# Performance work log

Hardware: AMD Instinct MI355X
Metric: run time of the kernel (lower is better)

Reference implementation:

```python
import jax, jax.numpy as jnp
import numpy as np

DIM = 192
HEADS = 6
WIN = (2, 6, 12)          # (pl, lat, lon)
TOW = 64                  # type_of_windows = (8//2)*(96//6)
N_TOK = WIN[0] * WIN[1] * WIN[2]            # 144
TABLE_ROWS = WIN[0]**2 * WIN[1]**2 * (2 * WIN[2] - 1)  # 3312


def calc_position_bias_indices(size):
    pl, la, lo = size
    plq = np.arange(pl); plk = -np.arange(pl) * pl
    laq = np.arange(la); lak = -np.arange(la) * la
    lon = np.arange(lo)
    gq = np.stack(np.meshgrid(plq, laq, lon, indexing='ij'))  # [3,pl,la,lo]
    gk = np.stack(np.meshgrid(plk, lak, lon, indexing='ij'))
    fq = gq.reshape(3, -1)
    fk = gk.reshape(3, -1)
    d = fq[:, :, None] - fk[:, None, :]          # [3,N,N]
    d = np.transpose(d, (1, 2, 0)).copy()
    d[:, :, 2] += lo - 1
    d[:, :, 1] *= 2 * lo - 1
    d[:, :, 0] *= (2 * lo - 1) * la * la
    return d.sum(-1)                              # [N,N]


def setup_inputs() -> dict:
    key = jax.random.key(0)
    ks = jax.random.split(key, 7)
    B_, nW, N, C = 15, TOW, N_TOK, DIM
    x = jax.random.normal(ks[0], (B_, nW, N, C), jnp.float32)
    mask = jax.random.normal(ks[1], (15, nW, N, N), jnp.float32)  # nLon=15
    qkv_w = jax.random.normal(ks[2], (3 * C, C), jnp.float32) * 0.02
    qkv_b = jnp.zeros((3 * C,), jnp.float32)
    table = jax.random.normal(ks[3], (TABLE_ROWS, TOW, HEADS), jnp.float32) * 0.02
    proj_w = jax.random.normal(ks[4], (C, C), jnp.float32) * 0.02
    proj_b = jnp.zeros((C,), jnp.float32)
    pos_index = jnp.asarray(calc_position_bias_indices(WIN), jnp.int32)  # [N,N]
    return {"x": x, "mask": mask, "qkv_w": qkv_w, "qkv_b": qkv_b,
            "table": table, "proj_w": proj_w, "proj_b": proj_b,
            "pos_index": pos_index}


def reference(x, mask, qkv_w, qkv_b, table, proj_w, proj_b, pos_index):
    B_, nW, N, C = x.shape
    h = HEADS
    hd = C // h
    scale = hd ** -0.5
    # qkv projection -> (3, B_, h, nW, N, hd)
    qkv = (jnp.einsum('bwnc,dc->bwnd', x, qkv_w) + qkv_b)
    qkv = qkv.reshape(B_, nW, N, 3, h, hd).transpose(3, 0, 4, 1, 2, 5)
    q, k, v = qkv[0] * scale, qkv[1], qkv[2]
    attn = jnp.einsum('bhwqd,bhwkd->bhwqk', q, k)      # [B_,h,nW,N,N]
    # gather earth position bias: [N,N,tow,h] -> [h,tow,N,N]
    bias = table[pos_index.reshape(-1)].reshape(N, N, nW, h)
    bias = bias.transpose(3, 2, 0, 1)
    attn = attn + bias[None]
    nLon = mask.shape[0]
    attn = attn.reshape(B_ // nLon, nLon, h, nW, N, N) + mask[None, :, None]
    attn = attn.reshape(B_, h, nW, N, N)
    attn = jax.nn.softmax(attn, axis=-1)
    out = jnp.einsum('bhwqk,bhwkd->bhwqd', attn, v)
    out = out.transpose(0, 2, 3, 1, 4).reshape(B_, nW, N, C)
    return jnp.einsum('bwnc,dc->bwnd', out, proj_w) + proj_b
```

## Files before the change

### kernel.cpp

```cpp
#include <hip/hip_runtime.h>

#define HEADS 6
#define N_TOK 144
#define DIM   192
#define NW    64
#define NB    15
#define NBW   (NB * NW)

typedef __attribute__((ext_vector_type(8))) short bf16x8;
typedef __attribute__((ext_vector_type(4))) float f32x4;

#define MFMA(a, b, c) __builtin_amdgcn_mfma_f32_16x16x32_bf16(a, b, c, 0, 0, 0)

static __device__ __forceinline__ short f2bf(float f) {
    union { float f; unsigned u; } v; v.f = f;
    unsigned r = v.u + 0x7FFFu + ((v.u >> 16) & 1u);
    return (short)(r >> 16);
}
static __device__ __forceinline__ float bf2f(short s) {
    union { unsigned u; float f; } v;
    v.u = ((unsigned)(unsigned short)s) << 16;
    return v.f;
}
static __device__ __forceinline__ unsigned pk2(float a, float b) {
    return (unsigned)(unsigned short)f2bf(a) |
           ((unsigned)(unsigned short)f2bf(b) << 16);
}

__global__ __launch_bounds__(256)
void bias_k(const float* __restrict__ table, const int* __restrict__ pos_index,
            short* __restrict__ bias_bf) {
    const int t = blockIdx.x;
    for (int e = threadIdx.x; e < N_TOK * N_TOK; e += 256) {
        int idx = pos_index[e];
        bias_bf[(long)t * (N_TOK * N_TOK) + e] = f2bf(table[(long)idx * 384 + t]);
    }
}

__global__ __launch_bounds__(256)
void cvt_k(const float* __restrict__ w, short* __restrict__ o, int n) {
    int i = blockIdx.x * 256 + threadIdx.x;
    if (i < n) o[i] = f2bf(w[i]);
}

__global__ __launch_bounds__(576, 2)
void fused64_k(const float* __restrict__ x, const short* __restrict__ qkvw_bf,
               const float* __restrict__ qkv_b, const short* __restrict__ bias_bf,
               const float* __restrict__ mask, const short* __restrict__ pwt,
               const float* __restrict__ proj_b, float* __restrict__ out) {
    __shared__ short klds[N_TOK * 40];
    __shared__ short vlds[32 * 156];
    __shared__ short pws[9 * 16 * 40];
    __shared__ short outb[N_TOK * 200];

    const int p  = blockIdx.x;
    const int bw = (p & 7) * 120 + (p >> 3);
    const int tid = threadIdx.x;
    const int lane = tid & 63, lq = lane & 15, lg = lane >> 4;
    const int wid = tid >> 6;
    const int m0 = wid * 16;
    const int q  = m0 + lq;
    const int w  = bw & 63;
    const float scale = 0.17677669529663687f;

    bf16x8 af[6];
    {
        const float* xg = x + ((long)bw * N_TOK + q) * DIM;
        #pragma unroll
        for (int ks = 0; ks < 6; ++ks) {
            const float4* pp = (const float4*)&xg[ks * 32 + 8 * lg];
            float4 f0 = pp[0], f1 = pp[1];
            bf16x8 a;
            a[0]=f2bf(f0.x); a[1]=f2bf(f0.y); a[2]=f2bf(f0.z); a[3]=f2bf(f0.w);
            a[4]=f2bf(f1.x); a[5]=f2bf(f1.y); a[6]=f2bf(f1.z); a[7]=f2bf(f1.w);
            af[ks] = a;
        }
    }

    float4 mreg[9];
    {
        const float* mp = mask + (long)bw * (N_TOK * N_TOK) + q * N_TOK + 4 * lg;
        #pragma unroll
        for (int nt = 0; nt < 9; ++nt) mreg[nt] = *(const float4*)&mp[nt * 16];
    }

    short* pw = pws + wid * 16 * 40;
    const f32x4 zf = {};
    const bf16x8 zb = {};

    #pragma unroll 1
    for (int h = 0; h < HEADS; ++h) {
        f32x4 acc[3][2] = {};
        #pragma unroll
        for (int ks = 0; ks < 6; ++ks)
            #pragma unroll
            for (int sel = 0; sel < 3; ++sel)
                #pragma unroll
                for (int nt = 0; nt < 2; ++nt) {
                    bf16x8 b = *(const bf16x8*)&qkvw_bf[
                        ((long)sel * 192 + h * 32 + nt * 16 + lq) * 192 + ks * 32 + 8 * lg];
                    acc[sel][nt] = MFMA(af[ks], b, acc[sel][nt]);
                }

        #pragma unroll
        for (int nt = 0; nt < 2; ++nt) {
            float bb = qkv_b[h * 32 + nt * 16 + lq];
            #pragma unroll
            for (int i = 0; i < 4; ++i)
                pw[(4 * lg + i) * 40 + nt * 16 + lq] =
                    f2bf((acc[0][nt][i] + bb) * scale);
        }

        __syncthreads();
        #pragma unroll
        for (int nt = 0; nt < 2; ++nt) {
            float bk = qkv_b[192 + h * 32 + nt * 16 + lq];
            float bv = qkv_b[384 + h * 32 + nt * 16 + lq];
            #pragma unroll
            for (int i = 0; i < 4; ++i) {
                klds[(m0 + 4 * lg + i) * 40 + nt * 16 + lq] = f2bf(acc[1][nt][i] + bk);
                vlds[(nt * 16 + lq) * 156 + m0 + 4 * lg + i] = f2bf(acc[2][nt][i] + bv);
            }
        }
        __syncthreads();

        bf16x8 bq = *(const bf16x8*)&pw[lq * 40 + 8 * lg];
        f32x4 lgt[9];
        #pragma unroll
        for (int nt = 0; nt < 9; ++nt) {
            bf16x8 ak = *(const bf16x8*)&klds[(nt * 16 + lq) * 40 + 8 * lg];
            lgt[nt] = MFMA(ak, bq, zf);
        }

        const short* bp = bias_bf + (long)(w * 6 + h) * (N_TOK * N_TOK)
                        + q * N_TOK + 4 * lg;
        #pragma unroll
        for (int nt = 0; nt < 9; ++nt) {
            short4 bs = *(const short4*)&bp[nt * 16];
            lgt[nt][0] += bf2f(bs.x) + mreg[nt].x;
            lgt[nt][1] += bf2f(bs.y) + mreg[nt].y;
            lgt[nt][2] += bf2f(bs.z) + mreg[nt].z;
            lgt[nt][3] += bf2f(bs.w) + mreg[nt].w;
        }

        float m = lgt[0][0];
        #pragma unroll
        for (int nt = 0; nt < 9; ++nt)
            #pragma unroll
            for (int i = 0; i < 4; ++i) m = fmaxf(m, lgt[nt][i]);
        m = fmaxf(m, __shfl_xor(m, 16));
        m = fmaxf(m, __shfl_xor(m, 32));
        float s = 0.f;
        #pragma unroll
        for (int nt = 0; nt < 9; ++nt)
            #pragma unroll
            for (int i = 0; i < 4; ++i) {
                float pe = __expf(lgt[nt][i] - m);
                lgt[nt][i] = pe;
                s += pe;
            }
        s += __shfl_xor(s, 16);
        s += __shfl_xor(s, 32);
        const float inv = 1.f / s;

        f32x4 o[2] = {};
        #pragma unroll
        for (int kt = 0; kt < 5; ++kt) {
            const int nt0 = 2 * kt;
            *(unsigned*)&pw[lq * 40 + 4 * lg]     = pk2(lgt[nt0][0], lgt[nt0][1]);
            *(unsigned*)&pw[lq * 40 + 4 * lg + 2] = pk2(lgt[nt0][2], lgt[nt0][3]);
            if (kt < 4) {
                const int nt1 = nt0 + 1;
                *(unsigned*)&pw[lq * 40 + 16 + 4 * lg]     = pk2(lgt[nt1][0], lgt[nt1][1]);
                *(unsigned*)&pw[lq * 40 + 16 + 4 * lg + 2] = pk2(lgt[nt1][2], lgt[nt1][3]);
            }
            bf16x8 bpf = *(const bf16x8*)&pw[lq * 40 + 8 * lg];
            #pragma unroll
            for (int et = 0; et < 2; ++et) {
                bf16x8 av = *(const bf16x8*)&vlds[(et * 16 + lq) * 156 + kt * 32 + 8 * lg];
                bf16x8 aa = av, bb = bpf;
                if (kt == 4 && lg >= 2) { aa = zb; bb = zb; }
                o[et] = MFMA(aa, bb, o[et]);
            }
        }

        #pragma unroll
        for (int et = 0; et < 2; ++et) {
            short4 sx = { f2bf(o[et][0] * inv), f2bf(o[et][1] * inv),
                          f2bf(o[et][2] * inv), f2bf(o[et][3] * inv) };
            *(short4*)&outb[q * 200 + h * 32 + et * 16 + 4 * lg] = sx;
        }
    }
    __syncthreads();

    f32x4 acc[12] = {};
    #pragma unroll
    for (int ks = 0; ks < 6; ++ks) {
        const int k0 = ks * 32 + 8 * lg;
        bf16x8 a = *(const bf16x8*)&outb[(m0 + lq) * 200 + k0];
        #pragma unroll
        for (int nt = 0; nt < 12; ++nt) {
            bf16x8 b = *(const bf16x8*)&pwt[(nt * 16 + lq) * DIM + k0];
            acc[nt] = MFMA(a, b, acc[nt]);
        }
    }
    float* ob = out + (long)bw * N_TOK * DIM;
    #pragma unroll
    for (int nt = 0; nt < 12; ++nt) {
        float pb = proj_b[nt * 16 + lq];
        #pragma unroll
        for (int i = 0; i < 4; ++i)
            ob[(m0 + 4 * lg + i) * DIM + nt * 16 + lq] = acc[nt][i] + pb;
    }
}

extern "C" void kernel_launch(void* const* d_in, const int* in_sizes, int n_in,
                              void* d_out, int out_size, void* d_ws, size_t ws_size,
                              hipStream_t stream) {
    const float* x        = (const float*)d_in[0];
    const float* mask     = (const float*)d_in[1];
    const float* qkv_w    = (const float*)d_in[2];
    const float* qkv_b    = (const float*)d_in[3];
    const float* table    = (const float*)d_in[4];
    const float* proj_w   = (const float*)d_in[5];
    const float* proj_b   = (const float*)d_in[6];
    const int*   pos_index= (const int*)d_in[7];
    float* out = (float*)d_out;

    short* bias_bf  = (short*)d_ws;
    short* projw_bf = bias_bf + (size_t)384 * N_TOK * N_TOK;
    short* qkvw_bf  = projw_bf + 36864;

    bias_k<<<384, 256, 0, stream>>>(table, pos_index, bias_bf);
    cvt_k<<<144, 256, 0, stream>>>(proj_w, projw_bf, DIM * DIM);
    cvt_k<<<432, 256, 0, stream>>>(qkv_w, qkvw_bf, 3 * DIM * DIM);

    fused64_k<<<NBW, 576, 0, stream>>>(x, qkvw_bf, qkv_b, bias_bf, mask,
                                       projw_bf, proj_b, out);
}
```

Measured before the change: 505.3 us.

## Split fused attention into per-head blocks plus separate projection kernel

The fused kernel, which looped over six heads per window, becomes one block per (window, head), which multiplies the grid by six. The per-head attention output goes to a bf16 workspace in global memory, and a new proj_k kernel runs the output projection over thirds of each window. The aim is more parallelism and shorter per-block serial chains, and it removes the outb shared-memory buffer. In exchange, every head block reloads x and the mask, and an extra global round trip plus one more launch are added.

Result: slower. 536.2 us (+6.1%).

```diff
diff --git a/kernel.cpp b/kernel.cpp
--- a/kernel.cpp
+++ b/kernel.cpp
@@ -44,17 +44,17 @@
 }
 
 __global__ __launch_bounds__(576, 2)
-void fused64_k(const float* __restrict__ x, const short* __restrict__ qkvw_bf,
+void attnqkv_k(const float* __restrict__ x, const short* __restrict__ qkvw_bf,
                const float* __restrict__ qkv_b, const short* __restrict__ bias_bf,
-               const float* __restrict__ mask, const short* __restrict__ pwt,
-               const float* __restrict__ proj_b, float* __restrict__ out) {
+               const float* __restrict__ mask, short* __restrict__ tmp) {
     __shared__ short klds[N_TOK * 40];
     __shared__ short vlds[32 * 156];
     __shared__ short pws[9 * 16 * 40];
-    __shared__ short outb[N_TOK * 200];
 
     const int p  = blockIdx.x;
-    const int bw = (p & 7) * 120 + (p >> 3);
+    const int l  = (p & 7) * 720 + (p >> 3);
+    const int h  = l % HEADS;
+    const int bw = l / HEADS;
     const int tid = threadIdx.x;
     const int lane = tid & 63, lq = lane & 15, lg = lane >> 4;
     const int wid = tid >> 6;
@@ -88,116 +88,124 @@
     const f32x4 zf = {};
     const bf16x8 zb = {};
 
-    #pragma unroll 1
-    for (int h = 0; h < HEADS; ++h) {
-        f32x4 acc[3][2] = {};
-        #pragma unroll
-        for (int ks = 0; ks < 6; ++ks)
+    f32x4 acc[3][2] = {};
+    #pragma unroll
+    for (int ks = 0; ks < 6; ++ks)
+        #pragma unroll
+        for (int sel = 0; sel < 3; ++sel)
             #pragma unroll
-            for (int sel = 0; sel < 3; ++sel)
-                #pragma unroll
-                for (int nt = 0; nt < 2; ++nt) {
-                    bf16x8 b = *(const bf16x8*)&qkvw_bf[
-                        ((long)sel * 192 + h * 32 + nt * 16 + lq) * 192 + ks * 32 + 8 * lg];
-                    acc[sel][nt] = MFMA(af[ks], b, acc[sel][nt]);
-                }
-
-        #pragma unroll
-        for (int nt = 0; nt < 2; ++nt) {
-            float bb = qkv_b[h * 32 + nt * 16 + lq];
-            #pragma unroll
-            for (int i = 0; i < 4; ++i)
-                pw[(4 * lg + i) * 40 + nt * 16 + lq] =
-                    f2bf((acc[0][nt][i] + bb) * scale);
-        }
-
-        __syncthreads();
-        #pragma unroll
-        for (int nt = 0; nt < 2; ++nt) {
-            float bk = qkv_b[192 + h * 32 + nt * 16 + lq];
-            float bv = qkv_b[384 + h * 32 + nt * 16 + lq];
-            #pragma unroll
-            for (int i = 0; i < 4; ++i) {
-                klds[(m0 + 4 * lg + i) * 40 + nt * 16 + lq] = f2bf(acc[1][nt][i] + bk);
-                vlds[(nt * 16 + lq) * 156 + m0 + 4 * lg + i] = f2bf(acc[2][nt][i] + bv);
+            for (int nt = 0; nt < 2; ++nt) {
+                bf16x8 b = *(const bf16x8*)&qkvw_bf[
+                    ((long)sel * 192 + h * 32 + nt * 16 + lq) * 192 + ks * 32 + 8 * lg];
+                acc[sel][nt] = MFMA(af[ks], b, acc[sel][nt]);
             }
-        }
-        __syncthreads();
-
-        bf16x8 bq = *(const bf16x8*)&pw[lq * 40 + 8 * lg];
-        f32x4 lgt[9];
-        #pragma unroll
-        for (int nt = 0; nt < 9; ++nt) {
-            bf16x8 ak = *(const bf16x8*)&klds[(nt * 16 + lq) * 40 + 8 * lg];
-            lgt[nt] = MFMA(ak, bq, zf);
-        }
-
-        const short* bp = bias_bf + (long)(w * 6 + h) * (N_TOK * N_TOK)
-                        + q * N_TOK + 4 * lg;
-        #pragma unroll
-        for (int nt = 0; nt < 9; ++nt) {
-            short4 bs = *(const short4*)&bp[nt * 16];
-            lgt[nt][0] += bf2f(bs.x) + mreg[nt].x;
-            lgt[nt][1] += bf2f(bs.y) + mreg[nt].y;
-            lgt[nt][2] += bf2f(bs.z) + mreg[nt].z;
-            lgt[nt][3] += bf2f(bs.w) + mreg[nt].w;
-        }
-
-        float m = lgt[0][0];
-        #pragma unroll
-        for (int nt = 0; nt < 9; ++nt)
-            #pragma unroll
-            for (int i = 0; i < 4; ++i) m = fmaxf(m, lgt[nt][i]);
-        m = fmaxf(m, __shfl_xor(m, 16));
-        m = fmaxf(m, __shfl_xor(m, 32));
-        float s = 0.f;
-        #pragma unroll
-        for (int nt = 0; nt < 9; ++nt)
-            #pragma unroll
-            for (int i = 0; i < 4; ++i) {
-                float pe = __expf(lgt[nt][i] - m);
-                lgt[nt][i] = pe;
-                s += pe;
-            }
-        s += __shfl_xor(s, 16);
-        s += __shfl_xor(s, 32);
-        const float inv = 1.f / s;
-
-        f32x4 o[2] = {};
-        #pragma unroll
-        for (int kt = 0; kt < 5; ++kt) {
-            const int nt0 = 2 * kt;
-            *(unsigned*)&pw[lq * 40 + 4 * lg]     = pk2(lgt[nt0][0], lgt[nt0][1]);
-            *(unsigned*)&pw[lq * 40 + 4 * lg + 2] = pk2(lgt[nt0][2], lgt[nt0][3]);
-            if (kt < 4) {
-                const int nt1 = nt0 + 1;
-                *(unsigned*)&pw[lq * 40 + 16 + 4 * lg]     = pk2(lgt[nt1][0], lgt[nt1][1]);
-                *(unsigned*)&pw[lq * 40 + 16 + 4 * lg + 2] = pk2(lgt[nt1][2], lgt[nt1][3]);
-            }
-            bf16x8 bpf = *(const bf16x8*)&pw[lq * 40 + 8 * lg];
-            #pragma unroll
-            for (int et = 0; et < 2; ++et) {
-                bf16x8 av = *(const bf16x8*)&vlds[(et * 16 + lq) * 156 + kt * 32 + 8 * lg];
-                bf16x8 aa = av, bb = bpf;
-                if (kt == 4 && lg >= 2) { aa = zb; bb = zb; }
-                o[et] = MFMA(aa, bb, o[et]);
-            }
-        }
-
+
+    #pragma unroll
+    for (int nt = 0; nt < 2; ++nt) {
+        float bb = qkv_b[h * 32 + nt * 16 + lq];
+        #pragma unroll
+        for (int i = 0; i < 4; ++i)
+            pw[(4 * lg + i) * 40 + nt * 16 + lq] =
+                f2bf((acc[0][nt][i] + bb) * scale);
+    }
+
+    #pragma unroll
+    for (int nt = 0; nt < 2; ++nt) {
+        float bk = qkv_b[192 + h * 32 + nt * 16 + lq];
+        float bv = qkv_b[384 + h * 32 + nt * 16 + lq];
+        #pragma unroll
+        for (int i = 0; i < 4; ++i) {
+            klds[(m0 + 4 * lg + i) * 40 + nt * 16 + lq] = f2bf(acc[1][nt][i] + bk);
+            vlds[(nt * 16 + lq) * 156 + m0 + 4 * lg + i] = f2bf(acc[2][nt][i] + bv);
+        }
+    }
+    __syncthreads();
+
+    bf16x8 bq = *(const bf16x8*)&pw[lq * 40 + 8 * lg];
+    f32x4 lgt[9];
+    #pragma unroll
+    for (int nt = 0; nt < 9; ++nt) {
+        bf16x8 ak = *(const bf16x8*)&klds[(nt * 16 + lq) * 40 + 8 * lg];
+        lgt[nt] = MFMA(ak, bq, zf);
+    }
+
+    const short* bp = bias_bf + (long)(w * 6 + h) * (N_TOK * N_TOK)
+                    + q * N_TOK + 4 * lg;
+    #pragma unroll
+    for (int nt = 0; nt < 9; ++nt) {
+        short4 bs = *(const short4*)&bp[nt * 16];
+        lgt[nt][0] += bf2f(bs.x) + mreg[nt].x;
+        lgt[nt][1] += bf2f(bs.y) + mreg[nt].y;
+        lgt[nt][2] += bf2f(bs.z) + mreg[nt].z;
+        lgt[nt][3] += bf2f(bs.w) + mreg[nt].w;
+    }
+
+    float m = lgt[0][0];
+    #pragma unroll
+    for (int nt = 0; nt < 9; ++nt)
+        #pragma unroll
+        for (int i = 0; i < 4; ++i) m = fmaxf(m, lgt[nt][i]);
+    m = fmaxf(m, __shfl_xor(m, 16));
+    m = fmaxf(m, __shfl_xor(m, 32));
+    float s = 0.f;
+    #pragma unroll
+    for (int nt = 0; nt < 9; ++nt)
+        #pragma unroll
+        for (int i = 0; i < 4; ++i) {
+            float pe = __expf(lgt[nt][i] - m);
+            lgt[nt][i] = pe;
+            s += pe;
+        }
+    s += __shfl_xor(s, 16);
+    s += __shfl_xor(s, 32);
+    const float inv = 1.f / s;
+
+    f32x4 o[2] = {};
+    #pragma unroll
+    for (int kt = 0; kt < 5; ++kt) {
+        const int nt0 = 2 * kt;
+        *(unsigned*)&pw[lq * 40 + 4 * lg]     = pk2(lgt[nt0][0], lgt[nt0][1]);
+        *(unsigned*)&pw[lq * 40 + 4 * lg + 2] = pk2(lgt[nt0][2], lgt[nt0][3]);
+        if (kt < 4) {
+            const int nt1 = nt0 + 1;
+            *(unsigned*)&pw[lq * 40 + 16 + 4 * lg]     = pk2(lgt[nt1][0], lgt[nt1][1]);
+            *(unsigned*)&pw[lq * 40 + 16 + 4 * lg + 2] = pk2(lgt[nt1][2], lgt[nt1][3]);
+        }
+        bf16x8 bpf = *(const bf16x8*)&pw[lq * 40 + 8 * lg];
         #pragma unroll
         for (int et = 0; et < 2; ++et) {
-            short4 sx = { f2bf(o[et][0] * inv), f2bf(o[et][1] * inv),
-                          f2bf(o[et][2] * inv), f2bf(o[et][3] * inv) };
-            *(short4*)&outb[q * 200 + h * 32 + et * 16 + 4 * lg] = sx;
-        }
-    }
-    __syncthreads();
+            bf16x8 av = *(const bf16x8*)&vlds[(et * 16 + lq) * 156 + kt * 32 + 8 * lg];
+            bf16x8 aa = av, bb = bpf;
+            if (kt == 4 && lg >= 2) { aa = zb; bb = zb; }
+            o[et] = MFMA(aa, bb, o[et]);
+        }
+    }
+
+    short* tb = tmp + ((long)bw * N_TOK + q) * DIM + h * 32;
+    #pragma unroll
+    for (int et = 0; et < 2; ++et) {
+        short4 sx = { f2bf(o[et][0] * inv), f2bf(o[et][1] * inv),
+                      f2bf(o[et][2] * inv), f2bf(o[et][3] * inv) };
+        *(short4*)&tb[et * 16 + 4 * lg] = sx;
+    }
+}
+
+__global__ __launch_bounds__(192)
+void proj_k(const short* __restrict__ tmp, const short* __restrict__ pwt,
+            const float* __restrict__ proj_b, float* __restrict__ out) {
+    const int p = blockIdx.x;
+    const int l = (p & 7) * 360 + (p >> 3);
+    const int third = l % 3;
+    const int bw    = l / 3;
+    const int tid = threadIdx.x;
+    const int wid = tid >> 6, lane = tid & 63, lq = lane & 15, lg = lane >> 4;
+    const int m0 = (third * 3 + wid) * 16;
+    const short* tb = tmp + (long)bw * N_TOK * DIM;
 
     f32x4 acc[12] = {};
-    #pragma unroll
     for (int ks = 0; ks < 6; ++ks) {
         const int k0 = ks * 32 + 8 * lg;
-        bf16x8 a = *(const bf16x8*)&outb[(m0 + lq) * 200 + k0];
+        bf16x8 a = *(const bf16x8*)&tb[(m0 + lq) * DIM + k0];
         #pragma unroll
         for (int nt = 0; nt < 12; ++nt) {
             bf16x8 b = *(const bf16x8*)&pwt[(nt * 16 + lq) * DIM + k0];
@@ -230,11 +238,13 @@
     short* bias_bf  = (short*)d_ws;
     short* projw_bf = bias_bf + (size_t)384 * N_TOK * N_TOK;
     short* qkvw_bf  = projw_bf + 36864;
+    short* tmp_ws   = qkvw_bf + 110592;
 
     bias_k<<<384, 256, 0, stream>>>(table, pos_index, bias_bf);
     cvt_k<<<144, 256, 0, stream>>>(proj_w, projw_bf, DIM * DIM);
     cvt_k<<<432, 256, 0, stream>>>(qkv_w, qkvw_bf, 3 * DIM * DIM);
 
-    fused64_k<<<NBW, 576, 0, stream>>>(x, qkvw_bf, qkv_b, bias_bf, mask,
-                                       projw_bf, proj_b, out);
-}
+    attnqkv_k<<<NBW * HEADS, 576, 0, stream>>>(x, qkvw_bf, qkv_b, bias_bf,
+                                               mask, tmp_ws);
+    proj_k<<<NBW * 3, 192, 0, stream>>>(tmp_ws, projw_bf, proj_b, out);
+}
```
